# Kernel tuning notes

Measured on AMD Instinct MI355X. Metric: run time of the kernel, lower is better.

## Reference

```python
import jax, jax.numpy as jnp
import numpy as np

N_NODES = 8      # objects per graph (fixed in source)
N_AT = 16        # anchors/targets vocab: 8 colors + 8 markers
H = 128          # n_hidden
BS = 16384


def _mlp(x, W1, b1, W2, b2):
    # layers.fully_connected default activation is relu; second layer linear.
    # dropout is identity in eval mode.
    return jax.nn.relu(x @ W1 + b1) @ W2 + b2


def _edges_and_segments(bs):
    # static edge list: all ordered pairs (i,j), i != j, per graph, offset per batch
    ii, jj = np.meshgrid(np.arange(N_NODES), np.arange(N_NODES), indexing='ij')
    m = ii != jj
    base = np.stack([ii[m], jj[m]], axis=1)                      # [56, 2]
    offs = (np.arange(bs) * N_NODES)[:, None, None]
    edges = (base[None] + offs).reshape(-1, 2).astype(np.int32)  # [bs*56, 2]
    seg_ids = np.repeat(np.arange(bs), N_NODES).astype(np.int32) # [bs*8]
    return jnp.asarray(edges), jnp.asarray(seg_ids)


def setup_inputs() -> dict:
    key = jax.random.key(0)
    ks = jax.random.split(key, 14)

    anchors = jax.random.randint(ks[0], (BS,), 0, N_AT)
    n_jumps = jax.random.randint(ks[1], (BS,), 0, N_NODES)
    positions = jax.random.uniform(ks[2], (BS, N_NODES, 2), dtype=jnp.float32)
    colors = jax.random.randint(ks[3], (BS, N_NODES), 0, 8)
    markers = jax.random.randint(ks[4], (BS, N_NODES), 8, 16)  # markers live in [8,16)

    def lin(k, fan_in, fan_out):
        return jax.random.normal(k, (fan_in, fan_out), dtype=jnp.float32) / np.sqrt(fan_in)

    d_in = 2 + 8 + 8 + N_AT + N_NODES  # pos + color_oh + marker_oh + question(16+8) = 42
    z = lambda n: jnp.zeros((n,), jnp.float32)
    return {
        'anchors': anchors, 'n_jumps': n_jumps, 'positions': positions,
        'colors': colors, 'markers': markers,
        'pre_W1': lin(ks[5], d_in, H),     'pre_b1': z(H),
        'pre_W2': lin(ks[6], H, H),        'pre_b2': z(H),
        'msg_W1': lin(ks[7], 2 * H + 1, H),'msg_b1': z(H),
        'msg_W2': lin(ks[8], H, H),        'msg_b2': z(H),
        'post_W1': lin(ks[9], 2 * H, H),   'post_b1': z(H),
        'post_W2': lin(ks[10], H, H),      'post_b2': z(H),
        'out_W1': lin(ks[11], H, H),       'out_b1': z(H),
        'out_W2': lin(ks[12], H, N_AT),    'out_b2': z(N_AT),
    }


def reference(anchors, n_jumps, positions, colors, markers,
              pre_W1, pre_b1, pre_W2, pre_b2,
              msg_W1, msg_b1, msg_W2, msg_b2,
              post_W1, post_b1, post_W2, post_b2,
              out_W1, out_b1, out_W2, out_b2):
    bs = positions.shape[0]
    edges, seg_ids = _edges_and_segments(bs)
    n_total = bs * N_NODES

    col_oh = jax.nn.one_hot(colors, 8, dtype=jnp.float32).reshape(n_total, 8)
    mrk_oh = jax.nn.one_hot(markers - 8, 8, dtype=jnp.float32).reshape(n_total, 8)
    pos = positions.reshape(n_total, 2)

    # pairwise euclidean distance per edge -> [E, 1]
    dp = pos[edges[:, 0]] - pos[edges[:, 1]]
    dist = jnp.sqrt(jnp.sum(dp * dp, axis=1, keepdims=True))

    # question broadcast to every node of its graph
    q = jnp.concatenate([jax.nn.one_hot(anchors, N_AT, dtype=jnp.float32),
                         jax.nn.one_hot(n_jumps, N_NODES, dtype=jnp.float32)], axis=1)
    q = q[seg_ids]  # [bs*8, 24]

    x0 = _mlp(jnp.concatenate([pos, col_oh, mrk_oh, q], axis=1),
              pre_W1, pre_b1, pre_W2, pre_b2)  # [bs*8, H]

    # one message-passing step: gather -> MLP -> scatter(segment_sum on source idx)
    mi = jnp.concatenate([x0[edges[:, 0]], x0[edges[:, 1]], dist], axis=1)  # [E, 257]
    msgs = _mlp(mi, msg_W1, msg_b1, msg_W2, msg_b2)                          # [E, H]
    upd = jax.ops.segment_sum(msgs, edges[:, 0], num_segments=n_total)       # [bs*8, H]

    x = _mlp(jnp.concatenate([upd, x0], axis=1), post_W1, post_b1, post_W2, post_b2)

    logits = jax.ops.segment_sum(x, seg_ids, num_segments=bs)  # [bs, H]
    logits = _mlp(logits, out_W1, out_b1, out_W2, out_b2)      # [bs, 16]
    return logits
```

## Files before the change

### kernel.cpp

```cpp
#include <hip/hip_runtime.h>

#define LROW 136
#define FSTR 72

typedef __bf16 bf16x8  __attribute__((ext_vector_type(8)));
typedef __bf16 bf16x2v __attribute__((ext_vector_type(2)));
typedef float  f32x4   __attribute__((ext_vector_type(4)));
typedef float  f32x2   __attribute__((ext_vector_type(2)));

#define MFMA16(a, b, c) __builtin_amdgcn_mfma_f32_16x16x32_bf16((a), (b), (c), 0, 0, 0)

__device__ __forceinline__ float bflo(unsigned v) { return __uint_as_float(v << 16); }
__device__ __forceinline__ float bfhi(unsigned v) { return __uint_as_float(v & 0xffff0000u); }

__device__ __forceinline__ unsigned short f2bf_u16(float f) {
  unsigned u = __float_as_uint(f);
  u += 0x7fffu + ((u >> 16) & 1u);
  return (unsigned short)(u >> 16);
}

__global__ void combine_weights(
    const float* __restrict__ pre_W1, const float* __restrict__ pre_b1,
    const float* __restrict__ pre_W2, const float* __restrict__ msg_W1,
    const float* __restrict__ msg_W2, const float* __restrict__ post_W1,
    const float* __restrict__ post_W2, const float* __restrict__ out_W1,
    const float* __restrict__ out_W2, const float* __restrict__ pre_b2,
    const float* __restrict__ msg_b1, const float* __restrict__ msg_b2,
    const float* __restrict__ post_b1, const float* __restrict__ post_b2,
    const float* __restrict__ out_b1,
    unsigned short* __restrict__ WabT, unsigned short* __restrict__ WdT,
    unsigned short* __restrict__ WcT, unsigned short* __restrict__ WoT,
    unsigned short* __restrict__ Wo2T, unsigned short* __restrict__ W1pT,
    float* __restrict__ vecs)
{
  __shared__ float part[256];
  const int b = blockIdx.x;
  const int t = threadIdx.x;
  if (b < 320) {
    const int p  = b >> 6;
    const int kp = b & 63;
    const int k  = kp * 2 + (t >> 7);
    const int n  = t & 127;
    const float* L; const float* R; unsigned short* O;
    if (p == 0)      { L = pre_W2;  R = msg_W1;             O = WabT; }
    else if (p == 1) { L = pre_W2;  R = msg_W1 + 128*128;   O = WabT + 128*128; }
    else if (p == 2) { L = pre_W2;  R = post_W1 + 128*128;  O = WdT; }
    else if (p == 3) { L = msg_W2;  R = post_W1;            O = WcT; }
    else             { L = post_W2; R = out_W1;             O = WoT; }
    const float* Lr = L + k * 128;
    float a0 = 0.f, a1 = 0.f, a2 = 0.f, a3 = 0.f;
    #pragma unroll 8
    for (int m = 0; m < 128; m += 4) {
      a0 = fmaf(Lr[m + 0], R[(m + 0) * 128 + n], a0);
      a1 = fmaf(Lr[m + 1], R[(m + 1) * 128 + n], a1);
      a2 = fmaf(Lr[m + 2], R[(m + 2) * 128 + n], a2);
      a3 = fmaf(Lr[m + 3], R[(m + 3) * 128 + n], a3);
    }
    O[n * 128 + k] = f2bf_u16((a0 + a1) + (a2 + a3));
  } else if (b == 320) {
    for (int idx = t; idx < 16 * 128; idx += 256) {
      int o = idx >> 7, k = idx & 127;
      Wo2T[o * 128 + k] = f2bf_u16(out_W2[k * 16 + o]);
    }
    if (t < 128) vecs[t] = msg_W1[256 * 128 + t];
    for (int idx = t; idx < 128 * 64; idx += 256) {
      int n = idx >> 6, k = idx & 63;
      float v = (k < 42) ? pre_W1[k * 128 + n] : (k == 42 ? pre_b1[n] : 0.f);
      W1pT[n * 64 + k] = f2bf_u16(v);
    }
  } else {
    const int n = t & 127;
    const int h = t >> 7;
    float s = 0.f;
    if (b == 321) {
      #pragma unroll 8
      for (int m = h * 64; m < h * 64 + 64; ++m)
        s = fmaf(pre_b2[m], msg_W1[m * 128 + n] + msg_W1[(128 + m) * 128 + n], s);
    } else if (b == 322) {
      #pragma unroll 8
      for (int m = h * 64; m < h * 64 + 64; ++m) {
        s = fmaf(7.f * msg_b2[m], post_W1[m * 128 + n], s);
        s = fmaf(pre_b2[m], post_W1[(128 + m) * 128 + n], s);
      }
    } else {
      #pragma unroll 8
      for (int m = h * 64; m < h * 64 + 64; ++m)
        s = fmaf(8.f * post_b2[m], out_W1[m * 128 + n], s);
    }
    part[t] = s;
    __syncthreads();
    if (t < 128) {
      float r = part[t] + part[t + 128];
      if (b == 321)      vecs[128 + t] = r + msg_b1[t];
      else if (b == 322) vecs[256 + t] = r + post_b1[t];
      else               vecs[384 + t] = r + out_b1[t];
    }
  }
}

__global__ void __launch_bounds__(256, 5) rrn_main(
    const int* __restrict__ anchors, const int* __restrict__ n_jumps,
    const float* __restrict__ positions, const int* __restrict__ colors,
    const int* __restrict__ markers,
    const __bf16* __restrict__ W1pT,
    const __bf16* __restrict__ WabT, const __bf16* __restrict__ WdT,
    const __bf16* __restrict__ WcT, const __bf16* __restrict__ WoT,
    const __bf16* __restrict__ Wo2T, const float* __restrict__ vecs,
    const float* __restrict__ out_b2, float* __restrict__ out)
{
  __shared__ __align__(16) char smem[20480];
  __bf16* featL = (__bf16*)(smem);
  __bf16* Ab    = (__bf16*)(smem);
  __bf16* h1    = (__bf16*)(smem + 8704);
  __bf16* Bb    = (__bf16*)(smem + 8704);
  __bf16* Sph   = (__bf16*)(smem + 8704);
  __bf16* hob   = (__bf16*)(smem + 13056);
  float*  dist  = (float*)(smem + 17408);
  float*  vec   = (float*)(smem + 18432);

  const int tid  = threadIdx.x;
  const int lane = tid & 63;
  const int w    = tid >> 6;
  const int l15  = lane & 15;
  const int quad = lane >> 4;
  const int colw = w * 32;
  const int crow = colw + 2 * l15;
  const int g0   = blockIdx.x * 4;
  const int n0   = blockIdx.x * 32;

  if (tid < 32) {
    uint4* rp = (uint4*)&featL[tid * FSTR];
    uint4 z4 = {0u, 0u, 0u, 0u};
    #pragma unroll
    for (int i = 0; i < 9; ++i) rp[i] = z4;
    int g = tid >> 3;
    float px = positions[(n0 + tid) * 2], py = positions[(n0 + tid) * 2 + 1];
    int c  = colors[n0 + tid], mk = markers[n0 + tid] - 8;
    int a  = anchors[g0 + g],  nj = n_jumps[g0 + g];
    __bf16* row = &featL[tid * FSTR];
    row[0] = (__bf16)px; row[1] = (__bf16)py;
    const __bf16 one = (__bf16)1.f;
    row[2 + c] = one; row[10 + mk] = one;
    row[18 + a] = one; row[34 + nj] = one;
    row[42] = one;
  }
  {
    int i = tid;
    int g = i >> 6, ii = (i >> 3) & 7, jj = i & 7;
    const float* pa = positions + (n0 + g * 8 + ii) * 2;
    const float* pb = positions + (n0 + g * 8 + jj) * 2;
    float dx = pa[0] - pb[0], dy = pa[1] - pb[1];
    dist[i] = sqrtf(dx * dx + dy * dy);
  }
  for (int i = tid; i < 512; i += 256) vec[i] = vecs[i];
  __syncthreads();

  {
    f32x4 acch[2][2];
    f32x4 zero = {0.f, 0.f, 0.f, 0.f};
    acch[0][0] = zero; acch[0][1] = zero; acch[1][0] = zero; acch[1][1] = zero;
    #pragma unroll
    for (int kb = 0; kb < 64; kb += 32) {
      const int ko = kb + quad * 8;
      bf16x8 fa[2], fb[2];
      fa[0] = *(const bf16x8*)&featL[(l15) * FSTR + ko];
      fa[1] = *(const bf16x8*)&featL[(16 + l15) * FSTR + ko];
      fb[0] = *(const bf16x8*)&W1pT[(crow) * 64 + ko];
      fb[1] = *(const bf16x8*)&W1pT[(crow + 1) * 64 + ko];
      #pragma unroll
      for (int mt = 0; mt < 2; ++mt) {
        acch[mt][0] = MFMA16(fa[mt], fb[0], acch[mt][0]);
        acch[mt][1] = MFMA16(fa[mt], fb[1], acch[mt][1]);
      }
    }
    #pragma unroll
    for (int mt = 0; mt < 2; ++mt)
      #pragma unroll
      for (int r = 0; r < 4; ++r) {
        bf16x2v o = { (__bf16)fmaxf(acch[mt][0][r], 0.f),
                      (__bf16)fmaxf(acch[mt][1][r], 0.f) };
        *(bf16x2v*)&h1[(mt * 16 + quad * 4 + r) * LROW + crow] = o;
      }
  }
  __syncthreads();

  {
    f32x4 accA[2][2];
    f32x4 zero = {0.f, 0.f, 0.f, 0.f};
    accA[0][0] = zero; accA[0][1] = zero; accA[1][0] = zero; accA[1][1] = zero;
    #pragma unroll
    for (int kb = 0; kb < 128; kb += 32) {
      const int ko = kb + quad * 8;
      bf16x8 fa[2], fb[2];
      fa[0] = *(const bf16x8*)&h1[(l15) * LROW + ko];
      fa[1] = *(const bf16x8*)&h1[(16 + l15) * LROW + ko];
      fb[0] = *(const bf16x8*)&WabT[(crow) * 128 + ko];
      fb[1] = *(const bf16x8*)&WabT[(crow + 1) * 128 + ko];
      accA[0][0] = MFMA16(fa[0], fb[0], accA[0][0]);
      accA[0][1] = MFMA16(fa[0], fb[1], accA[0][1]);
      accA[1][0] = MFMA16(fa[1], fb[0], accA[1][0]);
      accA[1][1] = MFMA16(fa[1], fb[1], accA[1][1]);
    }
    #pragma unroll
    for (int mt = 0; mt < 2; ++mt)
      #pragma unroll
      for (int r = 0; r < 4; ++r) {
        bf16x2v o = { (__bf16)accA[mt][0][r], (__bf16)accA[mt][1][r] };
        *(bf16x2v*)&Ab[(mt * 16 + quad * 4 + r) * LROW + crow] = o;
      }
  }

  f32x4 accD[2][2];
  {
    f32x4 accB[2][2];
    f32x4 zero = {0.f, 0.f, 0.f, 0.f};
    accB[0][0] = zero; accB[0][1] = zero; accB[1][0] = zero; accB[1][1] = zero;
    accD[0][0] = zero; accD[0][1] = zero; accD[1][0] = zero; accD[1][1] = zero;
    #pragma unroll
    for (int kb = 0; kb < 128; kb += 32) {
      const int ko = kb + quad * 8;
      bf16x8 fa[2], fb[2], fd[2];
      fa[0] = *(const bf16x8*)&h1[(l15) * LROW + ko];
      fa[1] = *(const bf16x8*)&h1[(16 + l15) * LROW + ko];
      fb[0] = *(const bf16x8*)&WabT[(128 + crow) * 128 + ko];
      fb[1] = *(const bf16x8*)&WabT[(128 + crow + 1) * 128 + ko];
      fd[0] = *(const bf16x8*)&WdT[(crow) * 128 + ko];
      fd[1] = *(const bf16x8*)&WdT[(crow + 1) * 128 + ko];
      accB[0][0] = MFMA16(fa[0], fb[0], accB[0][0]);
      accB[0][1] = MFMA16(fa[0], fb[1], accB[0][1]);
      accB[1][0] = MFMA16(fa[1], fb[0], accB[1][0]);
      accB[1][1] = MFMA16(fa[1], fb[1], accB[1][1]);
      accD[0][0] = MFMA16(fa[0], fd[0], accD[0][0]);
      accD[0][1] = MFMA16(fa[0], fd[1], accD[0][1]);
      accD[1][0] = MFMA16(fa[1], fd[0], accD[1][0]);
      accD[1][1] = MFMA16(fa[1], fd[1], accD[1][1]);
    }
    __syncthreads();
    #pragma unroll
    for (int mt = 0; mt < 2; ++mt)
      #pragma unroll
      for (int r = 0; r < 4; ++r) {
        bf16x2v o = { (__bf16)accB[mt][0][r], (__bf16)accB[mt][1][r] };
        *(bf16x2v*)&Bb[(mt * 16 + quad * 4 + r) * LROW + crow] = o;
      }
  }

  {
    const int c0 = colw + ((l15 & 8) << 1) + 2 * (l15 & 7);
    const f32x2 wv = { vec[c0], vec[c0 + 1] };
    const f32x2 cv = { vec[128 + c0], vec[128 + c0 + 1] };
    const f32x2 z2 = {0.f, 0.f};
    const int g = quad;
    f32x2 Bj[8];
    #pragma unroll
    for (int j = 0; j < 8; ++j) {
      unsigned vb = *(const unsigned*)&Bb[(g * 8 + j) * LROW + c0];
      Bj[j].x = bflo(vb); Bj[j].y = bfhi(vb);
    }
    #pragma unroll
    for (int i = 0; i < 8; ++i) {
      unsigned va = *(const unsigned*)&Ab[(g * 8 + i) * LROW + c0];
      f32x2 a = {bflo(va) + cv.x, bfhi(va) + cv.y};
      f32x2 s = z2;
      #pragma unroll
      for (int j = 0; j < 8; ++j) {
        if (j == i) continue;
        float d = dist[g * 64 + i * 8 + j];
        f32x2 d2 = {d, d};
        f32x2 t = __builtin_elementwise_fma(d2, wv, Bj[j]) + a;
        s += __builtin_elementwise_max(t, z2);
      }
      unsigned o = (unsigned)f2bf_u16(s.x) | ((unsigned)f2bf_u16(s.y) << 16);
      *(unsigned*)&Ab[(g * 8 + i) * LROW + c0] = o;
    }
  }
  __syncthreads();

  {
    #pragma unroll
    for (int rr = 0; rr < 3; ++rr)
      *(unsigned*)&Sph[(4 + quad * 3 + rr) * LROW + crow] = 0u;
    const __bf16* Sb = Ab;
    #pragma unroll
    for (int kb = 0; kb < 128; kb += 32) {
      const int ko = kb + quad * 8;
      bf16x8 fa[2], fc[2];
      fa[0] = *(const bf16x8*)&Sb[(l15) * LROW + ko];
      fa[1] = *(const bf16x8*)&Sb[(16 + l15) * LROW + ko];
      fc[0] = *(const bf16x8*)&WcT[(crow) * 128 + ko];
      fc[1] = *(const bf16x8*)&WcT[(crow + 1) * 128 + ko];
      accD[0][0] = MFMA16(fa[0], fc[0], accD[0][0]);
      accD[0][1] = MFMA16(fa[0], fc[1], accD[0][1]);
      accD[1][0] = MFMA16(fa[1], fc[0], accD[1][0]);
      accD[1][1] = MFMA16(fa[1], fc[1], accD[1][1]);
    }
    const f32x2 cpv = *(const f32x2*)&vec[256 + crow];
    #pragma unroll
    for (int mt = 0; mt < 2; ++mt) {
      f32x4 a0 = accD[mt][0];
      f32x4 a1 = accD[mt][1];
      float s0 = fmaxf(a0[0] + cpv.x, 0.f) + fmaxf(a0[1] + cpv.x, 0.f)
               + fmaxf(a0[2] + cpv.x, 0.f) + fmaxf(a0[3] + cpv.x, 0.f);
      float s1 = fmaxf(a1[0] + cpv.y, 0.f) + fmaxf(a1[1] + cpv.y, 0.f)
               + fmaxf(a1[2] + cpv.y, 0.f) + fmaxf(a1[3] + cpv.y, 0.f);
      s0 += __shfl_xor(s0, 16);
      s1 += __shfl_xor(s1, 16);
      int grow = mt * 2 + (lane >= 32 ? 1 : 0);
      if ((lane & 31) < 16) {
        bf16x2v o = { (__bf16)s0, (__bf16)s1 };
        *(bf16x2v*)&Sph[grow * LROW + crow] = o;
      }
    }
  }
  __syncthreads();

  {
    f32x4 acco[2];
    f32x4 zero = {0.f, 0.f, 0.f, 0.f};
    acco[0] = zero; acco[1] = zero;
    #pragma unroll
    for (int kb = 0; kb < 128; kb += 32) {
      const int ko = kb + quad * 8;
      bf16x8 fa = *(const bf16x8*)&Sph[l15 * LROW + ko];
      bf16x8 fb0 = *(const bf16x8*)&WoT[(crow) * 128 + ko];
      bf16x8 fb1 = *(const bf16x8*)&WoT[(crow + 1) * 128 + ko];
      acco[0] = MFMA16(fa, fb0, acco[0]);
      acco[1] = MFMA16(fa, fb1, acco[1]);
    }
    const f32x2 cov = *(const f32x2*)&vec[384 + crow];
    #pragma unroll
    for (int r = 0; r < 4; ++r) {
      bf16x2v o = { (__bf16)fmaxf(acco[0][r] + cov.x, 0.f),
                    (__bf16)fmaxf(acco[1][r] + cov.y, 0.f) };
      *(bf16x2v*)&hob[(quad * 4 + r) * LROW + crow] = o;
    }
  }
  __syncthreads();

  if (w == 0) {
    f32x4 accf = {0.f, 0.f, 0.f, 0.f};
    #pragma unroll
    for (int kb = 0; kb < 128; kb += 32) {
      const int ko = kb + quad * 8;
      bf16x8 fa  = *(const bf16x8*)&hob[l15 * LROW + ko];
      bf16x8 fbv = *(const bf16x8*)&Wo2T[l15 * 128 + ko];
      accf = MFMA16(fa, fbv, accf);
    }
    if (quad == 0) {
      float b2 = out_b2[l15];
      #pragma unroll
      for (int r = 0; r < 4; ++r)
        out[(g0 + r) * 16 + l15] = accf[r] + b2;
    }
  }
}

extern "C" void kernel_launch(void* const* d_in, const int* in_sizes, int n_in,
                              void* d_out, int out_size, void* d_ws, size_t ws_size,
                              hipStream_t stream) {
  const int*   anchors   = (const int*)d_in[0];
  const int*   n_jumps   = (const int*)d_in[1];
  const float* positions = (const float*)d_in[2];
  const int*   colors    = (const int*)d_in[3];
  const int*   markers   = (const int*)d_in[4];
  const float* pre_W1  = (const float*)d_in[5];
  const float* pre_b1  = (const float*)d_in[6];
  const float* pre_W2  = (const float*)d_in[7];
  const float* pre_b2  = (const float*)d_in[8];
  const float* msg_W1  = (const float*)d_in[9];
  const float* msg_b1  = (const float*)d_in[10];
  const float* msg_W2  = (const float*)d_in[11];
  const float* msg_b2  = (const float*)d_in[12];
  const float* post_W1 = (const float*)d_in[13];
  const float* post_b1 = (const float*)d_in[14];
  const float* post_W2 = (const float*)d_in[15];
  const float* post_b2 = (const float*)d_in[16];
  const float* out_W1  = (const float*)d_in[17];
  const float* out_b1  = (const float*)d_in[18];
  const float* out_W2  = (const float*)d_in[19];
  const float* out_b2  = (const float*)d_in[20];

  char* ws = (char*)d_ws;
  unsigned short* WabT = (unsigned short*)(ws);
  unsigned short* WdT  = (unsigned short*)(ws + 65536);
  unsigned short* WcT  = (unsigned short*)(ws + 98304);
  unsigned short* WoT  = (unsigned short*)(ws + 131072);
  unsigned short* Wo2T = (unsigned short*)(ws + 163840);
  float*          vecs = (float*)(ws + 167936);
  unsigned short* W1pT = (unsigned short*)(ws + 169984);

  const int BS = in_sizes[0];

  combine_weights<<<324, 256, 0, stream>>>(
      pre_W1, pre_b1, pre_W2, msg_W1, msg_W2, post_W1, post_W2, out_W1, out_W2,
      pre_b2, msg_b1, msg_b2, post_b1, post_b2, out_b1,
      WabT, WdT, WcT, WoT, Wo2T, W1pT, vecs);

  rrn_main<<<BS / 4, 256, 0, stream>>>(
      anchors, n_jumps, positions, colors, markers,
      (const __bf16*)W1pT,
      (const __bf16*)WabT, (const __bf16*)WdT, (const __bf16*)WcT,
      (const __bf16*)WoT, (const __bf16*)Wo2T, vecs, out_b2, (float*)d_out);
}
```

Baseline: 189.7 us.

## Process eight graphs per block with 512 threads and padded distance layout

Doubles the work per block from four to eight graphs, using 512 threads arranged as two row groups of four column warps. Each weight fragment loaded from global memory now feeds twice as many rows per block, so weight traffic per graph is cut roughly in half. The distance buffer gets a padded stride to reduce LDS bank conflicts, and zero-filling of the padded Sph rows moves into otherwise idle lanes. The cost is nearly double the shared memory per block and a 512-thread launch bound, which may lower occupancy or add register pressure, and the final output GEMM still runs on only half the warps.

```diff
diff --git a/kernel.cpp b/kernel.cpp
--- a/kernel.cpp
+++ b/kernel.cpp
@@ -2,6 +2,7 @@
 
 #define LROW 136
 #define FSTR 72
+#define DSTR 68
 
 typedef __bf16 bf16x8  __attribute__((ext_vector_type(8)));
 typedef __bf16 bf16x2v __attribute__((ext_vector_type(2)));
@@ -98,7 +99,7 @@
   }
 }
 
-__global__ void __launch_bounds__(256, 5) rrn_main(
+__global__ void __launch_bounds__(512, 6) rrn_main(
     const int* __restrict__ anchors, const int* __restrict__ n_jumps,
     const float* __restrict__ positions, const int* __restrict__ colors,
     const int* __restrict__ markers,
@@ -108,27 +109,30 @@
     const __bf16* __restrict__ Wo2T, const float* __restrict__ vecs,
     const float* __restrict__ out_b2, float* __restrict__ out)
 {
-  __shared__ __align__(16) char smem[20480];
+  __shared__ __align__(16) char smem[39040];
   __bf16* featL = (__bf16*)(smem);
   __bf16* Ab    = (__bf16*)(smem);
-  __bf16* h1    = (__bf16*)(smem + 8704);
-  __bf16* Bb    = (__bf16*)(smem + 8704);
-  __bf16* Sph   = (__bf16*)(smem + 8704);
-  __bf16* hob   = (__bf16*)(smem + 13056);
-  float*  dist  = (float*)(smem + 17408);
-  float*  vec   = (float*)(smem + 18432);
+  __bf16* h1    = (__bf16*)(smem + 17408);
+  __bf16* Bb    = (__bf16*)(smem + 17408);
+  __bf16* Sph   = (__bf16*)(smem + 17408);
+  __bf16* hob   = (__bf16*)(smem + 21760);
+  float*  dist  = (float*)(smem + 34816);
+  float*  vec   = (float*)(smem + 36992);
 
   const int tid  = threadIdx.x;
   const int lane = tid & 63;
   const int w    = tid >> 6;
+  const int wr   = w >> 2;
+  const int wc   = w & 3;
   const int l15  = lane & 15;
   const int quad = lane >> 4;
-  const int colw = w * 32;
+  const int colw = wc * 32;
   const int crow = colw + 2 * l15;
-  const int g0   = blockIdx.x * 4;
-  const int n0   = blockIdx.x * 32;
-
-  if (tid < 32) {
+  const int rbase = wr * 32;
+  const int g0   = blockIdx.x * 8;
+  const int n0   = blockIdx.x * 64;
+
+  if (tid < 64) {
     uint4* rp = (uint4*)&featL[tid * FSTR];
     uint4 z4 = {0u, 0u, 0u, 0u};
     #pragma unroll
@@ -150,9 +154,9 @@
     const float* pa = positions + (n0 + g * 8 + ii) * 2;
     const float* pb = positions + (n0 + g * 8 + jj) * 2;
     float dx = pa[0] - pb[0], dy = pa[1] - pb[1];
-    dist[i] = sqrtf(dx * dx + dy * dy);
-  }
-  for (int i = tid; i < 512; i += 256) vec[i] = vecs[i];
+    dist[g * DSTR + (i & 63)] = sqrtf(dx * dx + dy * dy);
+  }
+  vec[tid] = vecs[tid];
   __syncthreads();
 
   {
@@ -163,8 +167,8 @@
     for (int kb = 0; kb < 64; kb += 32) {
       const int ko = kb + quad * 8;
       bf16x8 fa[2], fb[2];
-      fa[0] = *(const bf16x8*)&featL[(l15) * FSTR + ko];
-      fa[1] = *(const bf16x8*)&featL[(16 + l15) * FSTR + ko];
+      fa[0] = *(const bf16x8*)&featL[(rbase + l15) * FSTR + ko];
+      fa[1] = *(const bf16x8*)&featL[(rbase + 16 + l15) * FSTR + ko];
       fb[0] = *(const bf16x8*)&W1pT[(crow) * 64 + ko];
       fb[1] = *(const bf16x8*)&W1pT[(crow + 1) * 64 + ko];
       #pragma unroll
@@ -179,7 +183,7 @@
       for (int r = 0; r < 4; ++r) {
         bf16x2v o = { (__bf16)fmaxf(acch[mt][0][r], 0.f),
                       (__bf16)fmaxf(acch[mt][1][r], 0.f) };
-        *(bf16x2v*)&h1[(mt * 16 + quad * 4 + r) * LROW + crow] = o;
+        *(bf16x2v*)&h1[(rbase + mt * 16 + quad * 4 + r) * LROW + crow] = o;
       }
   }
   __syncthreads();
@@ -192,8 +196,8 @@
     for (int kb = 0; kb < 128; kb += 32) {
       const int ko = kb + quad * 8;
       bf16x8 fa[2], fb[2];
-      fa[0] = *(const bf16x8*)&h1[(l15) * LROW + ko];
-      fa[1] = *(const bf16x8*)&h1[(16 + l15) * LROW + ko];
+      fa[0] = *(const bf16x8*)&h1[(rbase + l15) * LROW + ko];
+      fa[1] = *(const bf16x8*)&h1[(rbase + 16 + l15) * LROW + ko];
       fb[0] = *(const bf16x8*)&WabT[(crow) * 128 + ko];
       fb[1] = *(const bf16x8*)&WabT[(crow + 1) * 128 + ko];
       accA[0][0] = MFMA16(fa[0], fb[0], accA[0][0]);
@@ -206,7 +210,7 @@
       #pragma unroll
       for (int r = 0; r < 4; ++r) {
         bf16x2v o = { (__bf16)accA[mt][0][r], (__bf16)accA[mt][1][r] };
-        *(bf16x2v*)&Ab[(mt * 16 + quad * 4 + r) * LROW + crow] = o;
+        *(bf16x2v*)&Ab[(rbase + mt * 16 + quad * 4 + r) * LROW + crow] = o;
       }
   }
 
@@ -220,8 +224,8 @@
     for (int kb = 0; kb < 128; kb += 32) {
       const int ko = kb + quad * 8;
       bf16x8 fa[2], fb[2], fd[2];
-      fa[0] = *(const bf16x8*)&h1[(l15) * LROW + ko];
-      fa[1] = *(const bf16x8*)&h1[(16 + l15) * LROW + ko];
+      fa[0] = *(const bf16x8*)&h1[(rbase + l15) * LROW + ko];
+      fa[1] = *(const bf16x8*)&h1[(rbase + 16 + l15) * LROW + ko];
       fb[0] = *(const bf16x8*)&WabT[(128 + crow) * 128 + ko];
       fb[1] = *(const bf16x8*)&WabT[(128 + crow + 1) * 128 + ko];
       fd[0] = *(const bf16x8*)&WdT[(crow) * 128 + ko];
@@ -241,16 +245,16 @@
       #pragma unroll
       for (int r = 0; r < 4; ++r) {
         bf16x2v o = { (__bf16)accB[mt][0][r], (__bf16)accB[mt][1][r] };
-        *(bf16x2v*)&Bb[(mt * 16 + quad * 4 + r) * LROW + crow] = o;
-      }
-  }
-
-  {
-    const int c0 = colw + ((l15 & 8) << 1) + 2 * (l15 & 7);
+        *(bf16x2v*)&Bb[(rbase + mt * 16 + quad * 4 + r) * LROW + crow] = o;
+      }
+  }
+
+  {
+    const int c0 = colw + ((((l15 & 8) << 1) + 2 * (l15 & 7) + quad * 16) & 31);
     const f32x2 wv = { vec[c0], vec[c0 + 1] };
     const f32x2 cv = { vec[128 + c0], vec[128 + c0 + 1] };
     const f32x2 z2 = {0.f, 0.f};
-    const int g = quad;
+    const int g = wr * 4 + quad;
     f32x2 Bj[8];
     #pragma unroll
     for (int j = 0; j < 8; ++j) {
@@ -265,7 +269,7 @@
       #pragma unroll
       for (int j = 0; j < 8; ++j) {
         if (j == i) continue;
-        float d = dist[g * 64 + i * 8 + j];
+        float d = dist[g * DSTR + i * 8 + j];
         f32x2 d2 = {d, d};
         f32x2 t = __builtin_elementwise_fma(d2, wv, Bj[j]) + a;
         s += __builtin_elementwise_max(t, z2);
@@ -277,16 +281,13 @@
   __syncthreads();
 
   {
-    #pragma unroll
-    for (int rr = 0; rr < 3; ++rr)
-      *(unsigned*)&Sph[(4 + quad * 3 + rr) * LROW + crow] = 0u;
     const __bf16* Sb = Ab;
     #pragma unroll
     for (int kb = 0; kb < 128; kb += 32) {
       const int ko = kb + quad * 8;
       bf16x8 fa[2], fc[2];
-      fa[0] = *(const bf16x8*)&Sb[(l15) * LROW + ko];
-      fa[1] = *(const bf16x8*)&Sb[(16 + l15) * LROW + ko];
+      fa[0] = *(const bf16x8*)&Sb[(rbase + l15) * LROW + ko];
+      fa[1] = *(const bf16x8*)&Sb[(rbase + 16 + l15) * LROW + ko];
       fc[0] = *(const bf16x8*)&WcT[(crow) * 128 + ko];
       fc[1] = *(const bf16x8*)&WcT[(crow + 1) * 128 + ko];
       accD[0][0] = MFMA16(fa[0], fc[0], accD[0][0]);
@@ -305,16 +306,18 @@
                + fmaxf(a1[2] + cpv.y, 0.f) + fmaxf(a1[3] + cpv.y, 0.f);
       s0 += __shfl_xor(s0, 16);
       s1 += __shfl_xor(s1, 16);
-      int grow = mt * 2 + (lane >= 32 ? 1 : 0);
+      int grow = wr * 4 + mt * 2 + (lane >= 32 ? 1 : 0);
       if ((lane & 31) < 16) {
         bf16x2v o = { (__bf16)s0, (__bf16)s1 };
         *(bf16x2v*)&Sph[grow * LROW + crow] = o;
+      } else {
+        *(unsigned*)&Sph[(8 + grow) * LROW + crow] = 0u;
       }
     }
   }
   __syncthreads();
 
-  {
+  if (w < 4) {
     f32x4 acco[2];
     f32x4 zero = {0.f, 0.f, 0.f, 0.f};
     acco[0] = zero; acco[1] = zero;
@@ -346,11 +349,13 @@
       bf16x8 fbv = *(const bf16x8*)&Wo2T[l15 * 128 + ko];
       accf = MFMA16(fa, fbv, accf);
     }
-    if (quad == 0) {
+    if (quad < 2) {
       float b2 = out_b2[l15];
       #pragma unroll
-      for (int r = 0; r < 4; ++r)
-        out[(g0 + r) * 16 + l15] = accf[r] + b2;
+      for (int r = 0; r < 4; ++r) {
+        int row = quad * 4 + r;
+        out[(g0 + row) * 16 + l15] = accf[r] + b2;
+      }
     }
   }
 }
@@ -396,7 +401,7 @@
       pre_b2, msg_b1, msg_b2, post_b1, post_b2, out_b1,
       WabT, WdT, WcT, WoT, Wo2T, W1pT, vecs);
 
-  rrn_main<<<BS / 4, 256, 0, stream>>>(
+  rrn_main<<<BS / 8, 512, 0, stream>>>(
       anchors, n_jumps, positions, colors, markers,
       (const __bf16*)W1pT,
       (const __bf16*)WabT, (const __bf16*)WdT, (const __bf16*)WcT,
```

After: 184.2 us. 1.03x faster.
